# Kernel optimization log

Measured on AMD Instinct MI355X. Metric: run time of the kernel, lower is better.

Reference implementation:

```python
import jax, jax.numpy as jnp
import numpy as np

B, S, IN, OUT = 16, 512, 512, 256
D, H, L, DFF = 1024, 16, 6, 2048
HD = D // H
SCALE = HD ** -0.5
HID = 256  # fc1/fc2 hidden size


def setup_inputs() -> dict:
    key = jax.random.key(0)
    ks = jax.random.split(key, 40)
    g = lambda i, shape, s=0.02: (jax.random.normal(ks[i], shape, jnp.float32) * s)
    z = lambda shape: jnp.zeros(shape, jnp.float32)
    o = lambda shape: jnp.ones(shape, jnp.float32)
    vec = jnp.zeros((B, S), jnp.int32).at[:, 0].set(1)  # one-hot rows (assert-only arg)
    return {
        "x": jax.random.normal(ks[0], (B, S, IN), jnp.float32),
        "xm": jax.random.uniform(ks[1], (B, S), jnp.float32),
        "vecSelector": vec,
        "proj_w": g(2, (IN, D)), "proj_b": z((D,)),
        "pos": g(3, (S, D)),
        "qw": g(4, (L, D, D)), "qb": z((L, D)),
        "kw": g(5, (L, D, D)), "kb": z((L, D)),
        "vw": g(6, (L, D, D)), "vb": z((L, D)),
        "ow": g(7, (L, D, D)), "ob": z((L, D)),
        "ln1_g": o((L, D)), "ln1_b": z((L, D)),
        "ln2_g": o((L, D)), "ln2_b": z((L, D)),
        "w1": g(8, (L, D, DFF)), "b1": z((L, DFF)),
        "w2": g(9, (L, DFF, D)), "b2": z((L, D)),
        "fc1_w": g(10, (D, HID)), "fc1_b": z((HID,)),
        "fc2_w": g(11, (HID, HID)), "fc2_b": z((HID,)),
        "fc3_w": g(12, (HID, OUT)), "fc3_b": z((OUT,)),
    }


def _ln(x, g, b, eps=1e-5):
    m = jnp.mean(x, -1, keepdims=True)
    v = jnp.mean((x - m) ** 2, -1, keepdims=True)
    return (x - m) * jax.lax.rsqrt(v + eps) * g + b


def reference(x, xm, vecSelector, proj_w, proj_b, pos, qw, qb, kw, kb, vw, vb,
              ow, ob, ln1_g, ln1_b, ln2_g, ln2_b, w1, b1, w2, b2,
              fc1_w, fc1_b, fc2_w, fc2_b, fc3_w, fc3_b):
    # linear_proj + positional encoding (pos[:, :d_model] == pos)
    h = x @ proj_w + proj_b + pos  # (B,S,D)
    # key padding mask: whole batch rows masked where xm.sum(-1)==0
    skpm = jnp.broadcast_to((jnp.sum(xm, -1) == 0)[:, None], (B, S))  # (B,S) bool
    neg_inf = jnp.float32(-jnp.inf)
    for i in range(L):
        q = (h @ qw[i] + qb[i]) * SCALE
        k = h @ kw[i] + kb[i]
        v = h @ vw[i] + vb[i]
        q = q.reshape(B, S, H, HD)
        k = k.reshape(B, S, H, HD)
        v = v.reshape(B, S, H, HD)
        sc = jnp.einsum('bthd,bshd->bhts', q, k)  # (B,H,T,S)
        sc = jnp.where(skpm[:, None, None, :], neg_inf, sc)
        # safe_softmax: clamp to [-10,10] THEN softmax (-inf -> -10)
        aw = jax.nn.softmax(jnp.clip(sc, -10.0, 10.0), axis=-1)
        ao = jnp.einsum('bhts,bshd->bthd', aw, v).reshape(B, S, D)
        ao = ao @ ow[i] + ob[i]
        # forward hook: clamp + softmax over embed dim
        ao = jax.nn.softmax(jnp.clip(ao, -10.0, 10.0), axis=-1)
        # torch _sa_block's `[0]` slices batch dim of the raw tensor -> (S,D),
        # broadcast-added to every batch row
        sa = ao[0]
        h = _ln(h + sa[None, :, :], ln1_g[i], ln1_b[i])
        ff = jax.nn.relu(h @ w1[i] + b1[i]) @ w2[i] + b2[i]
        h = _ln(h + ff, ln2_g[i], ln2_b[i])
    out = h @ fc1_w + fc1_b
    for _ in range(5):
        out = out @ fc2_w + fc2_b
    out = out @ fc3_w + fc3_b  # (B,S,OUT)
    return out
```

## Files before the change

### kernel.cpp

```cpp
#include <hip/hip_runtime.h>
#include <hip/hip_bf16.h>

using bf16 = __hip_bfloat16;
typedef __attribute__((ext_vector_type(8))) short short8v;
typedef __attribute__((ext_vector_type(4))) float floatx4;

constexpr int Bc = 16, Sc = 512, INc = 512, OUTc = 256;
constexpr int Dc = 1024, Hc = 16, Lc = 6, DFFc = 2048, HIDc = 256;
constexpr float SCALEc = 0.125f;
constexpr int QKVS = 3072;

__device__ inline ushort f2b(float f) {
    union { float f; unsigned u; } v; v.f = f;
    unsigned r = (v.u + 0x7FFF + ((v.u >> 16) & 1)) >> 16;
    return (ushort)r;
}
__device__ inline float b2f(ushort b) {
    union { unsigned u; float f; } v; v.u = ((unsigned)b) << 16;
    return v.f;
}
__device__ inline float ldf(const float* p) { return *p; }
__device__ inline float ldf(const ushort* p) { return b2f(*p); }

__device__ inline void gll16(const ushort* g, ushort* l) {
    __builtin_amdgcn_global_load_lds(
        (const __attribute__((address_space(1))) unsigned int*)g,
        (__attribute__((address_space(3))) unsigned int*)l, 16, 0, 0);
}

__device__ inline float blockSum256(float v) {
    __shared__ float tmp[4];
#pragma unroll
    for (int o = 32; o > 0; o >>= 1) v += __shfl_xor(v, o, 64);
    int w = threadIdx.x >> 6;
    __syncthreads();
    if ((threadIdx.x & 63) == 0) tmp[w] = v;
    __syncthreads();
    return tmp[0] + tmp[1] + tmp[2] + tmp[3];
}
__device__ inline float blockMax256(float v) {
    __shared__ float tmp[4];
#pragma unroll
    for (int o = 32; o > 0; o >>= 1) v = fmaxf(v, __shfl_xor(v, o, 64));
    int w = threadIdx.x >> 6;
    __syncthreads();
    if ((threadIdx.x & 63) == 0) tmp[w] = v;
    __syncthreads();
    return fmaxf(fmaxf(tmp[0], tmp[1]), fmaxf(tmp[2], tmp[3]));
}

__global__ __launch_bounds__(256) void mask_k(const float* __restrict__ xm, float* __restrict__ flag) {
    float s = xm[threadIdx.x] + xm[threadIdx.x + 256];
    s = blockSum256(s);
    if (threadIdx.x == 0) flag[0] = (s == 0.f) ? 1.f : 0.f;
}

__global__ __launch_bounds__(256) void transp_k(const float* __restrict__ W, ushort* __restrict__ Wt,
                                                int K, int N, float wscale) {
    __shared__ float Ls[64][65];
    const int t = threadIdx.x;
    const int n0 = blockIdx.x * 64, k0 = blockIdx.y * 64;
    const int kr = t >> 4, n4 = (t & 15) * 4;
#pragma unroll
    for (int p = 0; p < 4; ++p) {
        float4 v = *(const float4*)&W[(size_t)(k0 + kr + p * 16) * N + n0 + n4];
        Ls[kr + p * 16][n4 + 0] = v.x; Ls[kr + p * 16][n4 + 1] = v.y;
        Ls[kr + p * 16][n4 + 2] = v.z; Ls[kr + p * 16][n4 + 3] = v.w;
    }
    __syncthreads();
    const int nr = t >> 4, k4 = (t & 15) * 4;
#pragma unroll
    for (int p = 0; p < 4; ++p) {
        ushort4 o;
        o.x = f2b(Ls[k4 + 0][nr + p * 16] * wscale); o.y = f2b(Ls[k4 + 1][nr + p * 16] * wscale);
        o.z = f2b(Ls[k4 + 2][nr + p * 16] * wscale); o.w = f2b(Ls[k4 + 3][nr + p * 16] * wscale);
        *(ushort4*)&Wt[(size_t)(n0 + nr + p * 16) * K + k0 + k4] = o;
    }
}

__global__ __launch_bounds__(256) void transp4_k(const float* __restrict__ qw, const float* __restrict__ kw,
                                                 const float* __restrict__ vw, const float* __restrict__ ow,
                                                 ushort* __restrict__ Wt) {
    const int z = blockIdx.z;
    const float* W = (z == 0) ? qw : (z == 1) ? kw : (z == 2) ? vw : ow;
    const float wscale = (z == 0) ? SCALEc : 1.f;
    ushort* dst = Wt + (size_t)z * Dc * Dc;
    __shared__ float Ls[64][65];
    const int t = threadIdx.x;
    const int n0 = blockIdx.x * 64, k0 = blockIdx.y * 64;
    const int kr = t >> 4, n4 = (t & 15) * 4;
#pragma unroll
    for (int p = 0; p < 4; ++p) {
        float4 v = *(const float4*)&W[(size_t)(k0 + kr + p * 16) * Dc + n0 + n4];
        Ls[kr + p * 16][n4 + 0] = v.x; Ls[kr + p * 16][n4 + 1] = v.y;
        Ls[kr + p * 16][n4 + 2] = v.z; Ls[kr + p * 16][n4 + 3] = v.w;
    }
    __syncthreads();
    const int nr = t >> 4, k4 = (t & 15) * 4;
#pragma unroll
    for (int p = 0; p < 4; ++p) {
        ushort4 o;
        o.x = f2b(Ls[k4 + 0][nr + p * 16] * wscale); o.y = f2b(Ls[k4 + 1][nr + p * 16] * wscale);
        o.z = f2b(Ls[k4 + 2][nr + p * 16] * wscale); o.w = f2b(Ls[k4 + 3][nr + p * 16] * wscale);
        *(ushort4*)&dst[(size_t)(n0 + nr + p * 16) * Dc + k0 + k4] = o;
    }
}

__device__ inline void ld16(const float* s, ushort* d) {
#pragma unroll
    for (int i = 0; i < 4; ++i) {
        float4 v = *(const float4*)(s + i * 4);
        d[i * 4 + 0] = f2b(v.x); d[i * 4 + 1] = f2b(v.y);
        d[i * 4 + 2] = f2b(v.z); d[i * 4 + 3] = f2b(v.w);
    }
}

template <typename TA, int ACT, bool ADDPOS, int OMODE>
__global__ __launch_bounds__(256) void mgemm_k(
    const TA* __restrict__ A, const ushort* __restrict__ Bt,
    const float* __restrict__ bias, const float* __restrict__ pos,
    float* __restrict__ Cf, ushort* __restrict__ Cb,
    int M, int N, int K, float scale)
{
    __shared__ __align__(16) ushort As[128 * 64];
    __shared__ __align__(16) ushort Bs[128 * 64];
    const int tid = threadIdx.x;
    const int nx = gridDim.x;
    const int nwg = nx * gridDim.y;
    int d = blockIdx.x + blockIdx.y * nx;
    if ((nwg & 7) == 0) d = (d & 7) * (nwg >> 3) + (d >> 3);
    const int m0 = (d / nx) * 128, n0 = (d % nx) * 128;
    const int lane = tid & 63, wv = tid >> 6;
    const int wm = (wv >> 1) * 64, wn = (wv & 1) * 64;
    floatx4 acc[4][4] = {};

    const int rA8 = lane >> 3, cch = lane & 7;
    const int srow = tid >> 2, scg = tid & 3;

    for (int k0 = 0; k0 < K; k0 += 64) {
#pragma unroll
        for (int p = 0; p < 4; ++p) {
            const int r = wv * 32 + p * 8 + rA8;
            const int cs = (cch ^ (r & 7)) * 8;
            gll16(&Bt[(size_t)(n0 + r) * K + k0 + cs], &Bs[(wv * 32 + p * 8) * 64]);
        }
        if constexpr (sizeof(TA) == 2) {
#pragma unroll
            for (int p = 0; p < 4; ++p) {
                const int r = wv * 32 + p * 8 + rA8;
                const int cs = (cch ^ (r & 7)) * 8;
                gll16((const ushort*)&A[(size_t)(m0 + r) * K + k0 + cs], &As[(wv * 32 + p * 8) * 64]);
            }
        } else {
#pragma unroll
            for (int p = 0; p < 2; ++p) {
                const int r = srow + p * 64;
                __align__(16) ushort ta[16];
                ld16(&A[(size_t)(m0 + r) * K + k0 + scg * 16], ta);
                const int base = r * 64, sw = (r & 7) * 8;
                *(short8v*)&As[base + ((scg * 16 + 0) ^ sw)] = *(short8v*)&ta[0];
                *(short8v*)&As[base + ((scg * 16 + 8) ^ sw)] = *(short8v*)&ta[8];
            }
        }
        __syncthreads();
#pragma unroll
        for (int s = 0; s < 2; ++s) {
            short8v af[4], bf_[4];
            const int kg = s * 32 + (lane >> 4) * 8;
#pragma unroll
            for (int f = 0; f < 4; ++f) {
                const int ra = wm + f * 16 + (lane & 15);
                af[f] = *(const short8v*)&As[ra * 64 + (kg ^ ((ra & 7) * 8))];
                const int rb = wn + f * 16 + (lane & 15);
                bf_[f] = *(const short8v*)&Bs[rb * 64 + (kg ^ ((rb & 7) * 8))];
            }
#pragma unroll
            for (int i = 0; i < 4; ++i)
#pragma unroll
                for (int j = 0; j < 4; ++j)
                    acc[i][j] = __builtin_amdgcn_mfma_f32_16x16x32_bf16(af[i], bf_[j], acc[i][j], 0, 0, 0);
        }
        __syncthreads();
    }

    const int cc = lane & 15, rr4 = (lane >> 4) * 4;
#pragma unroll
    for (int i = 0; i < 4; ++i) {
#pragma unroll
        for (int j = 0; j < 4; ++j) {
            const int col = n0 + wn + j * 16 + cc;
            const float bsv = bias[col];
#pragma unroll
            for (int q = 0; q < 4; ++q) {
                const int row = m0 + wm + i * 16 + rr4 + q;
                float v = acc[i][j][q] + bsv;
                if (ADDPOS) v += pos[(size_t)(row & (Sc - 1)) * N + col];
                v *= scale;
                if (ACT == 1) v = fmaxf(v, 0.f);
                if (OMODE == 0) Cf[(size_t)row * N + col] = v;
                else if (OMODE == 1) Cb[(size_t)row * N + col] = f2b(v);
                else { Cf[(size_t)row * N + col] = v; Cb[(size_t)row * N + col] = f2b(v); }
            }
        }
    }
}

__global__ __launch_bounds__(256) void fattn_k(
    const float* __restrict__ qkv, ushort* __restrict__ ao, const float* __restrict__ flag)
{
    const int hh = blockIdx.y;
    const int t0 = blockIdx.x * 32;
    __shared__ __align__(16) ushort Qs[32 * 64];
    __shared__ __align__(16) ushort Ks[64 * 64];
    __shared__ float Vs[64][68];
    __shared__ float Ps[32][68];
    __shared__ float rs[4][32];
    const int tid = threadIdx.x;
    const int lane = tid & 63, wv = tid >> 6;
    const bool msk = flag[0] > 0.5f;

    {
        const int r = tid >> 3, c = tid & 7;
        const float* src = &qkv[(size_t)(t0 + r) * QKVS + hh * 64 + c * 8];
        float4 v0 = *(const float4*)src, v1 = *(const float4*)(src + 4);
        __align__(16) ushort tmp[8] = {f2b(v0.x), f2b(v0.y), f2b(v0.z), f2b(v0.w),
                                       f2b(v1.x), f2b(v1.y), f2b(v1.z), f2b(v1.w)};
        *(short8v*)&Qs[r * 64 + ((c * 8) ^ ((r & 7) * 8))] = *(short8v*)tmp;
    }
    if (tid < 128) ((float*)rs)[tid] = 0.f;

    float o[8] = {};
    const int pq = tid >> 3, pd = (tid & 7) * 8;

    for (int s0 = 0; s0 < Sc; s0 += 64) {
        __syncthreads();
        {
            const int vr = tid >> 2, vc = (tid & 3) * 16;
            const float* vsrc = &qkv[(size_t)(s0 + vr) * QKVS + 2048 + hh * 64 + vc];
#pragma unroll
            for (int u = 0; u < 4; ++u)
                *(float4*)&Vs[vr][vc + u * 4] = *(const float4*)(vsrc + u * 4);
#pragma unroll
            for (int u = 0; u < 2; ++u) {
                const int task = tid + u * 256;
                const int kr = task >> 3, kc = task & 7;
                const float* ksrc = &qkv[(size_t)(s0 + kr) * QKVS + 1024 + hh * 64 + kc * 8];
                float4 a = *(const float4*)ksrc, b = *(const float4*)(ksrc + 4);
                __align__(16) ushort tmp[8] = {f2b(a.x), f2b(a.y), f2b(a.z), f2b(a.w),
                                               f2b(b.x), f2b(b.y), f2b(b.z), f2b(b.w)};
                *(short8v*)&Ks[kr * 64 + ((kc * 8) ^ ((kr & 7) * 8))] = *(short8v*)tmp;
            }
        }
        __syncthreads();
        floatx4 pacc[2] = {};
#pragma unroll
        for (int i = 0; i < 2; ++i)
#pragma unroll
            for (int s = 0; s < 2; ++s) {
                const int kg = s * 32 + (lane >> 4) * 8;
                const int ra = 16 * i + (lane & 15);
                short8v aq = *(const short8v*)&Qs[ra * 64 + (kg ^ ((ra & 7) * 8))];
                const int rb = 16 * wv + (lane & 15);
                short8v bk = *(const short8v*)&Ks[rb * 64 + (kg ^ ((rb & 7) * 8))];
                pacc[i] = __builtin_amdgcn_mfma_f32_16x16x32_bf16(aq, bk, pacc[i], 0, 0, 0);
            }
        const int cc = lane & 15, rr4 = (lane >> 4) * 4;
#pragma unroll
        for (int i = 0; i < 2; ++i)
#pragma unroll
            for (int q = 0; q < 4; ++q) {
                float v = fminf(fmaxf(pacc[i][q], -10.f), 10.f);
                if (msk) v = -10.f;
                float e = __expf(v - 10.f);
                Ps[16 * i + rr4 + q][wv * 16 + cc] = e;
                float rsum = e;
                rsum += __shfl_xor(rsum, 1, 64);
                rsum += __shfl_xor(rsum, 2, 64);
                rsum += __shfl_xor(rsum, 4, 64);
                rsum += __shfl_xor(rsum, 8, 64);
                if (cc == 0) rs[wv][16 * i + rr4 + q] += rsum;
            }
        __syncthreads();
#pragma unroll 8
        for (int ss = 0; ss < 64; ++ss) {
            float p = Ps[pq][ss];
#pragma unroll
            for (int u = 0; u < 8; ++u) o[u] += p * Vs[ss][pd + u];
        }
    }
    __syncthreads();
    float inv = 1.f / (rs[0][pq] + rs[1][pq] + rs[2][pq] + rs[3][pq]);
#pragma unroll
    for (int u = 0; u < 8; ++u)
        ao[(size_t)(t0 + pq) * Dc + hh * 64 + pd + u] = f2b(o[u] * inv);
}

template <typename TA, int ACT, bool ADDPOS, bool OUT_BF16, bool HASB>
__global__ __launch_bounds__(256) void gemm_k(
    const TA* __restrict__ A, const float* __restrict__ W,
    const float* __restrict__ bias, const float* __restrict__ pos,
    float* __restrict__ Cf, bf16* __restrict__ Cb,
    int M, int N, int K, float scale)
{
    __shared__ float As[16][68];
    __shared__ float Ws[16][68];
    const int tid = threadIdx.x;
    const int m0 = blockIdx.y * 64, n0 = blockIdx.x * 64;
    const int ty = tid >> 4, tx = tid & 15;
    float c[4][4] = {};

    const int ka = tid & 15, mb = tid >> 4;
    const int nw = tid & 63, kb = tid >> 6;

    for (int k0 = 0; k0 < K; k0 += 16) {
#pragma unroll
        for (int j = 0; j < 4; ++j) {
            int m = mb + 16 * j;
            As[ka][m] = ldf(&A[(size_t)(m0 + m) * K + k0 + ka]);
        }
#pragma unroll
        for (int j = 0; j < 4; ++j) {
            int k = kb + 4 * j;
            Ws[k][nw] = W[(size_t)(k0 + k) * N + n0 + nw];
        }
        __syncthreads();
#pragma unroll
        for (int k = 0; k < 16; ++k) {
            float4 av = *(const float4*)&As[k][ty * 4];
            float4 wv = *(const float4*)&Ws[k][tx * 4];
            float a[4] = {av.x, av.y, av.z, av.w};
            float w[4] = {wv.x, wv.y, wv.z, wv.w};
#pragma unroll
            for (int i = 0; i < 4; ++i)
#pragma unroll
                for (int j = 0; j < 4; ++j) c[i][j] += a[i] * w[j];
        }
        __syncthreads();
    }

#pragma unroll
    for (int i = 0; i < 4; ++i) {
        int m = m0 + ty * 4 + i;
#pragma unroll
        for (int j = 0; j < 4; ++j) {
            int n = n0 + tx * 4 + j;
            float v = c[i][j] + (HASB ? bias[n] : 0.f);
            if (ADDPOS) v += pos[(size_t)(m & (Sc - 1)) * N + n];
            v *= scale;
            if (ACT == 1) v = fmaxf(v, 0.f);
            if (OUT_BF16) Cb[(size_t)m * N + n] = __float2bfloat16(v);
            else          Cf[(size_t)m * N + n] = v;
        }
    }
}

__global__ __launch_bounds__(256) void biaschain_k(
    const float* __restrict__ fc1b, const float* __restrict__ fc2w, const float* __restrict__ fc2b,
    const float* __restrict__ fc3w, const float* __restrict__ fc3b, float* __restrict__ bc)
{
    __shared__ float vs[256];
    const int t = threadIdx.x;
    float v = fc1b[t];
    for (int r = 0; r < 5; ++r) {
        vs[t] = v; __syncthreads();
        float s = fc2b[t];
#pragma unroll 8
        for (int k = 0; k < 256; ++k) s += vs[k] * fc2w[k * 256 + t];
        v = s; __syncthreads();
    }
    vs[t] = v; __syncthreads();
    float s = fc3b[t];
#pragma unroll 8
    for (int k = 0; k < 256; ++k) s += vs[k] * fc3w[k * 256 + t];
    bc[t] = s;
}

__global__ __launch_bounds__(256) void qkvbias_k(
    const float* __restrict__ qb, const float* __restrict__ kb, const float* __restrict__ vb,
    float* __restrict__ o)
{
    int i = blockIdx.x * 256 + threadIdx.x;
    float v = (i < 1024) ? qb[i] * SCALEc : ((i < 2048) ? kb[i - 1024] : vb[i - 2048]);
    o[i] = v;
}

__global__ __launch_bounds__(256) void softmax_k(
    const float* __restrict__ in, float* __restrict__ out, int ncols, int doclip)
{
    const int row = blockIdx.x;
    const float* ip = in + (size_t)row * ncols;
    float* op = out + (size_t)row * ncols;
    const int nj = ncols >> 8;
    float r[4];
    float mx = -1e30f;
    for (int j = 0; j < nj; ++j) {
        float v = ip[threadIdx.x + 256 * j];
        if (doclip) v = fminf(fmaxf(v, -10.f), 10.f);
        r[j] = v;
        mx = fmaxf(mx, v);
    }
    mx = blockMax256(mx);
    float s = 0.f;
    for (int j = 0; j < nj; ++j) { r[j] = expf(r[j] - mx); s += r[j]; }
    s = blockSum256(s);
    float inv = 1.f / s;
    for (int j = 0; j < nj; ++j) op[threadIdx.x + 256 * j] = r[j] * inv;
}

template <bool BCAST, typename TADD>
__global__ __launch_bounds__(256) void add_ln_k(
    ushort* __restrict__ hb, const TADD* __restrict__ add,
    const float* __restrict__ g, const float* __restrict__ b)
{
    const int row = blockIdx.x;
    const TADD* ap = BCAST ? add + (size_t)(row & (Sc - 1)) * Dc : add + (size_t)row * Dc;
    ushort* hp = hb + (size_t)row * Dc;
    const int tid = threadIdx.x;
    const int c0 = tid * 4;
    ushort4 hv = *(const ushort4*)&hp[c0];
    float x[4] = {b2f(hv.x), b2f(hv.y), b2f(hv.z), b2f(hv.w)};
#pragma unroll
    for (int j = 0; j < 4; ++j) x[j] += ldf(&ap[c0 + j]);
    float s = x[0] + x[1] + x[2] + x[3];
    float mean = blockSum256(s) * (1.f / (float)Dc);
    float vsum = 0.f;
#pragma unroll
    for (int j = 0; j < 4; ++j) { float d = x[j] - mean; vsum += d * d; }
    float var = blockSum256(vsum) * (1.f / (float)Dc);
    float inv = rsqrtf(var + 1e-5f);
    float4 gv = *(const float4*)&g[c0];
    float4 bv = *(const float4*)&b[c0];
    ushort4 ov;
    ov.x = f2b((x[0] - mean) * inv * gv.x + bv.x);
    ov.y = f2b((x[1] - mean) * inv * gv.y + bv.y);
    ov.z = f2b((x[2] - mean) * inv * gv.z + bv.z);
    ov.w = f2b((x[3] - mean) * inv * gv.w + bv.w);
    *(ushort4*)&hp[c0] = ov;
}

extern "C" void kernel_launch(void* const* d_in, const int* in_sizes, int n_in,
                              void* d_out, int out_size, void* d_ws, size_t ws_size,
                              hipStream_t stream)
{
    const float* x      = (const float*)d_in[0];
    const float* xm     = (const float*)d_in[1];
    const float* proj_w = (const float*)d_in[3];
    const float* proj_b = (const float*)d_in[4];
    const float* pos    = (const float*)d_in[5];
    const float* qw     = (const float*)d_in[6];
    const float* qb     = (const float*)d_in[7];
    const float* kw     = (const float*)d_in[8];
    const float* kb     = (const float*)d_in[9];
    const float* vw     = (const float*)d_in[10];
    const float* vb     = (const float*)d_in[11];
    const float* ow     = (const float*)d_in[12];
    const float* obias  = (const float*)d_in[13];
    const float* ln1g   = (const float*)d_in[14];
    const float* ln1b   = (const float*)d_in[15];
    const float* ln2g   = (const float*)d_in[16];
    const float* ln2b   = (const float*)d_in[17];
    const float* w1     = (const float*)d_in[18];
    const float* b1     = (const float*)d_in[19];
    const float* w2     = (const float*)d_in[20];
    const float* b2     = (const float*)d_in[21];
    const float* fc1w   = (const float*)d_in[22];
    const float* fc1b   = (const float*)d_in[23];
    const float* fc2w   = (const float*)d_in[24];
    const float* fc2b   = (const float*)d_in[25];
    const float* fc3w   = (const float*)d_in[26];
    const float* fc3b   = (const float*)d_in[27];

    float* ws = (float*)d_ws;
    const size_t HSZ = (size_t)Bc * Sc * Dc;
    ushort* hb  = (ushort*)ws;
    ushort* ffu = (ushort*)(ws + HSZ / 2);
    float* rgA  = ws + HSZ;
    float* rgB  = ws + 2 * HSZ;
    float* flag = ws + 3 * HSZ;

    float* qkvf  = rgA;
    ushort* aovu = (ushort*)(rgA + 1572864);
    float* obv   = rgA + 1835008;
    float* qkvb  = rgA + 2359296;
    ushort* midu = (ushort*)rgA;

    ushort* Wt = (ushort*)rgB;

    float* W2  = rgA;
    float* W4  = rgA + 65536;
    float* W5  = rgA + 131072;
    float* C1  = rgA + 196608;
    float* Wc  = rgA + 458752;
    float* bcv = rgA + 720896;

    const int MR = Bc * Sc;

    mask_k<<<1, 256, 0, stream>>>(xm, flag);

    transp_k<<<dim3(Dc / 64, INc / 64), 256, 0, stream>>>(proj_w, Wt, INc, Dc, 1.f);
    mgemm_k<float, 0, true, 1><<<dim3(Dc / 128, MR / 128), 256, 0, stream>>>(
        x, Wt, proj_b, pos, nullptr, hb, MR, Dc, INc, 1.f);

    for (int l = 0; l < Lc; ++l) {
        const float* qw_l = qw + (size_t)l * Dc * Dc; const float* qb_l = qb + l * Dc;
        const float* kw_l = kw + (size_t)l * Dc * Dc; const float* kb_l = kb + l * Dc;
        const float* vw_l = vw + (size_t)l * Dc * Dc; const float* vb_l = vb + l * Dc;
        const float* ow_l = ow + (size_t)l * Dc * Dc; const float* ob_l = obias + l * Dc;
        const float* w1_l = w1 + (size_t)l * Dc * DFFc; const float* b1_l = b1 + l * DFFc;
        const float* w2_l = w2 + (size_t)l * DFFc * Dc; const float* b2_l = b2 + l * Dc;

        transp4_k<<<dim3(Dc / 64, Dc / 64, 4), 256, 0, stream>>>(qw_l, kw_l, vw_l, ow_l, Wt);
        qkvbias_k<<<12, 256, 0, stream>>>(qb_l, kb_l, vb_l, qkvb);
        mgemm_k<ushort, 0, false, 0><<<dim3(QKVS / 128, Sc / 128), 256, 0, stream>>>(
            hb, Wt, qkvb, nullptr, qkvf, nullptr, Sc, QKVS, Dc, 1.f);
        fattn_k<<<dim3(Sc / 32, Hc), 256, 0, stream>>>(qkvf, aovu, flag);
        mgemm_k<ushort, 0, false, 0><<<dim3(Dc / 128, Sc / 128), 256, 0, stream>>>(
            aovu, Wt + (size_t)3 * Dc * Dc, ob_l, nullptr, obv, nullptr, Sc, Dc, Dc, 1.f);
        softmax_k<<<Sc, 256, 0, stream>>>(obv, obv, Dc, 1);
        add_ln_k<true, float><<<MR, 256, 0, stream>>>(hb, obv, ln1g + l * Dc, ln1b + l * Dc);

        transp_k<<<dim3(DFFc / 64, Dc / 64), 256, 0, stream>>>(w1_l, Wt, Dc, DFFc, 1.f);
        mgemm_k<ushort, 1, false, 1><<<dim3(DFFc / 128, MR / 128), 256, 0, stream>>>(
            hb, Wt, b1_l, nullptr, nullptr, midu, MR, DFFc, Dc, 1.f);
        transp_k<<<dim3(Dc / 64, DFFc / 64), 256, 0, stream>>>(w2_l, Wt, DFFc, Dc, 1.f);
        mgemm_k<ushort, 0, false, 1><<<dim3(Dc / 128, MR / 128), 256, 0, stream>>>(
            midu, Wt, b2_l, nullptr, nullptr, ffu, MR, Dc, DFFc, 1.f);
        add_ln_k<false, ushort><<<MR, 256, 0, stream>>>(hb, ffu, ln2g + l * Dc, ln2b + l * Dc);
    }

    gemm_k<float, 0, false, false, false><<<dim3(4, 4), 256, 0, stream>>>(
        fc2w, fc2w, nullptr, nullptr, W2, nullptr, HIDc, HIDc, HIDc, 1.f);
    gemm_k<float, 0, false, false, false><<<dim3(4, 4), 256, 0, stream>>>(
        W2, W2, nullptr, nullptr, W4, nullptr, HIDc, HIDc, HIDc, 1.f);
    gemm_k<float, 0, false, false, false><<<dim3(4, 4), 256, 0, stream>>>(
        W4, fc2w, nullptr, nullptr, W5, nullptr, HIDc, HIDc, HIDc, 1.f);
    gemm_k<float, 0, false, false, false><<<dim3(4, 16), 256, 0, stream>>>(
        fc1w, W5, nullptr, nullptr, C1, nullptr, Dc, HIDc, HIDc, 1.f);
    gemm_k<float, 0, false, false, false><<<dim3(4, 16), 256, 0, stream>>>(
        C1, fc3w, nullptr, nullptr, Wc, nullptr, Dc, HIDc, HIDc, 1.f);
    biaschain_k<<<1, 256, 0, stream>>>(fc1b, fc2w, fc2b, fc3w, fc3b, bcv);
    transp_k<<<dim3(HIDc / 64, Dc / 64), 256, 0, stream>>>(Wc, Wt, Dc, HIDc, 1.f);
    mgemm_k<ushort, 0, false, 0><<<dim3(HIDc / 128, MR / 128), 256, 0, stream>>>(
        hb, Wt, bcv, nullptr, (float*)d_out, nullptr, MR, HIDc, Dc, 1.f);
}
```

Before: 1.403 ms.

## Batch all-layer weight transposes, bf16 QKV output, fuse softmax into add+LN

When the workspace is large enough, all six layers' weights are transposed to bf16 in one up-front launch, and the QKV biases for every layer are built in a single kernel. The QKV GEMM now writes bf16, so attention loads K/Q directly without converting. The output-projection softmax is folded into the residual add plus LayerNorm kernel. This cuts launch count, intermediate traffic and per-layer transpose overhead, at the cost of more workspace and a path that depends on the workspace size.

```diff
diff --git a/kernel.cpp b/kernel.cpp
--- a/kernel.cpp
+++ b/kernel.cpp
@@ -9,6 +9,7 @@
 constexpr int Dc = 1024, Hc = 16, Lc = 6, DFFc = 2048, HIDc = 256;
 constexpr float SCALEc = 0.125f;
 constexpr int QKVS = 3072;
+constexpr size_t LSLOT = 8388608;
 
 __device__ inline ushort f2b(float f) {
     union { float f; unsigned u; } v; v.f = f;
@@ -78,20 +79,31 @@
     }
 }
 
-__global__ __launch_bounds__(256) void transp4_k(const float* __restrict__ qw, const float* __restrict__ kw,
-                                                 const float* __restrict__ vw, const float* __restrict__ ow,
-                                                 ushort* __restrict__ Wt) {
+__global__ __launch_bounds__(256) void transpall_k(
+    const float* __restrict__ qw, const float* __restrict__ kw, const float* __restrict__ vw,
+    const float* __restrict__ ow, const float* __restrict__ w1, const float* __restrict__ w2,
+    ushort* __restrict__ Wt, int l0, size_t lstride)
+{
     const int z = blockIdx.z;
-    const float* W = (z == 0) ? qw : (z == 1) ? kw : (z == 2) ? vw : ow;
-    const float wscale = (z == 0) ? SCALEc : 1.f;
-    ushort* dst = Wt + (size_t)z * Dc * Dc;
+    const int l = l0 + z / 6, m = z % 6;
+    ushort* slot = Wt + (size_t)(z / 6) * lstride;
+    const float* W; ushort* dst; int K, N; float wscale = 1.f;
+    switch (m) {
+        case 0: W = qw + (size_t)l * Dc * Dc; K = Dc; N = Dc; dst = slot; wscale = SCALEc; break;
+        case 1: W = kw + (size_t)l * Dc * Dc; K = Dc; N = Dc; dst = slot + 1048576; break;
+        case 2: W = vw + (size_t)l * Dc * Dc; K = Dc; N = Dc; dst = slot + 2097152; break;
+        case 3: W = ow + (size_t)l * Dc * Dc; K = Dc; N = Dc; dst = slot + 3145728; break;
+        case 4: W = w1 + (size_t)l * Dc * DFFc; K = Dc; N = DFFc; dst = slot + 4194304; break;
+        default: W = w2 + (size_t)l * DFFc * Dc; K = DFFc; N = Dc; dst = slot + 6291456; break;
+    }
+    if (blockIdx.x >= N / 64 || blockIdx.y >= K / 64) return;
     __shared__ float Ls[64][65];
     const int t = threadIdx.x;
     const int n0 = blockIdx.x * 64, k0 = blockIdx.y * 64;
     const int kr = t >> 4, n4 = (t & 15) * 4;
 #pragma unroll
     for (int p = 0; p < 4; ++p) {
-        float4 v = *(const float4*)&W[(size_t)(k0 + kr + p * 16) * Dc + n0 + n4];
+        float4 v = *(const float4*)&W[(size_t)(k0 + kr + p * 16) * N + n0 + n4];
         Ls[kr + p * 16][n4 + 0] = v.x; Ls[kr + p * 16][n4 + 1] = v.y;
         Ls[kr + p * 16][n4 + 2] = v.z; Ls[kr + p * 16][n4 + 3] = v.w;
     }
@@ -102,7 +114,7 @@
         ushort4 o;
         o.x = f2b(Ls[k4 + 0][nr + p * 16] * wscale); o.y = f2b(Ls[k4 + 1][nr + p * 16] * wscale);
         o.z = f2b(Ls[k4 + 2][nr + p * 16] * wscale); o.w = f2b(Ls[k4 + 3][nr + p * 16] * wscale);
-        *(ushort4*)&dst[(size_t)(n0 + nr + p * 16) * Dc + k0 + k4] = o;
+        *(ushort4*)&dst[(size_t)(n0 + nr + p * 16) * K + k0 + k4] = o;
     }
 }
 
@@ -206,7 +218,7 @@
 }
 
 __global__ __launch_bounds__(256) void fattn_k(
-    const float* __restrict__ qkv, ushort* __restrict__ ao, const float* __restrict__ flag)
+    const ushort* __restrict__ qkv, ushort* __restrict__ ao, const float* __restrict__ flag)
 {
     const int hh = blockIdx.y;
     const int t0 = blockIdx.x * 32;
@@ -221,11 +233,8 @@
 
     {
         const int r = tid >> 3, c = tid & 7;
-        const float* src = &qkv[(size_t)(t0 + r) * QKVS + hh * 64 + c * 8];
-        float4 v0 = *(const float4*)src, v1 = *(const float4*)(src + 4);
-        __align__(16) ushort tmp[8] = {f2b(v0.x), f2b(v0.y), f2b(v0.z), f2b(v0.w),
-                                       f2b(v1.x), f2b(v1.y), f2b(v1.z), f2b(v1.w)};
-        *(short8v*)&Qs[r * 64 + ((c * 8) ^ ((r & 7) * 8))] = *(short8v*)tmp;
+        short8v q = *(const short8v*)&qkv[(size_t)(t0 + r) * QKVS + hh * 64 + c * 8];
+        *(short8v*)&Qs[r * 64 + ((c * 8) ^ ((r & 7) * 8))] = q;
     }
     if (tid < 128) ((float*)rs)[tid] = 0.f;
 
@@ -236,19 +245,19 @@
         __syncthreads();
         {
             const int vr = tid >> 2, vc = (tid & 3) * 16;
-            const float* vsrc = &qkv[(size_t)(s0 + vr) * QKVS + 2048 + hh * 64 + vc];
-#pragma unroll
-            for (int u = 0; u < 4; ++u)
-                *(float4*)&Vs[vr][vc + u * 4] = *(const float4*)(vsrc + u * 4);
+            const ushort* vsrc = &qkv[(size_t)(s0 + vr) * QKVS + 2048 + hh * 64 + vc];
+            short8v v0 = *(const short8v*)vsrc, v1 = *(const short8v*)(vsrc + 8);
+#pragma unroll
+            for (int u = 0; u < 8; ++u) {
+                Vs[vr][vc + u] = b2f((ushort)v0[u]);
+                Vs[vr][vc + 8 + u] = b2f((ushort)v1[u]);
+            }
 #pragma unroll
             for (int u = 0; u < 2; ++u) {
                 const int task = tid + u * 256;
                 const int kr = task >> 3, kc = task & 7;
-                const float* ksrc = &qkv[(size_t)(s0 + kr) * QKVS + 1024 + hh * 64 + kc * 8];
-                float4 a = *(const float4*)ksrc, b = *(const float4*)(ksrc + 4);
-                __align__(16) ushort tmp[8] = {f2b(a.x), f2b(a.y), f2b(a.z), f2b(a.w),
-                                               f2b(b.x), f2b(b.y), f2b(b.z), f2b(b.w)};
-                *(short8v*)&Ks[kr * 64 + ((kc * 8) ^ ((kr & 7) * 8))] = *(short8v*)tmp;
+                short8v kvv = *(const short8v*)&qkv[(size_t)(s0 + kr) * QKVS + 1024 + hh * 64 + kc * 8];
+                *(short8v*)&Ks[kr * 64 + ((kc * 8) ^ ((kr & 7) * 8))] = kvv;
             }
         }
         __syncthreads();
@@ -375,36 +384,55 @@
     bc[t] = s;
 }
 
-__global__ __launch_bounds__(256) void qkvbias_k(
+__global__ __launch_bounds__(256) void qkvbiasall_k(
     const float* __restrict__ qb, const float* __restrict__ kb, const float* __restrict__ vb,
     float* __restrict__ o)
 {
     int i = blockIdx.x * 256 + threadIdx.x;
-    float v = (i < 1024) ? qb[i] * SCALEc : ((i < 2048) ? kb[i - 1024] : vb[i - 2048]);
+    int l = i / QKVS, j = i - l * QKVS;
+    float v = (j < 1024) ? qb[l * Dc + j] * SCALEc
+            : (j < 2048) ? kb[l * Dc + j - 1024] : vb[l * Dc + j - 2048];
     o[i] = v;
 }
 
-__global__ __launch_bounds__(256) void softmax_k(
-    const float* __restrict__ in, float* __restrict__ out, int ncols, int doclip)
+__global__ __launch_bounds__(256) void smaddln_k(
+    ushort* __restrict__ hb, const float* __restrict__ obv,
+    const float* __restrict__ g, const float* __restrict__ b)
 {
     const int row = blockIdx.x;
-    const float* ip = in + (size_t)row * ncols;
-    float* op = out + (size_t)row * ncols;
-    const int nj = ncols >> 8;
-    float r[4];
+    const float* op = obv + (size_t)(row & (Sc - 1)) * Dc;
+    ushort* hp = hb + (size_t)row * Dc;
+    const int c0 = threadIdx.x * 4;
+    float4 ov = *(const float4*)&op[c0];
+    float r[4] = {ov.x, ov.y, ov.z, ov.w};
     float mx = -1e30f;
-    for (int j = 0; j < nj; ++j) {
-        float v = ip[threadIdx.x + 256 * j];
-        if (doclip) v = fminf(fmaxf(v, -10.f), 10.f);
-        r[j] = v;
-        mx = fmaxf(mx, v);
-    }
+#pragma unroll
+    for (int j = 0; j < 4; ++j) { r[j] = fminf(fmaxf(r[j], -10.f), 10.f); mx = fmaxf(mx, r[j]); }
     mx = blockMax256(mx);
     float s = 0.f;
-    for (int j = 0; j < nj; ++j) { r[j] = expf(r[j] - mx); s += r[j]; }
+#pragma unroll
+    for (int j = 0; j < 4; ++j) { r[j] = __expf(r[j] - mx); s += r[j]; }
     s = blockSum256(s);
-    float inv = 1.f / s;
-    for (int j = 0; j < nj; ++j) op[threadIdx.x + 256 * j] = r[j] * inv;
+    float sinv = 1.f / s;
+    ushort4 hv = *(const ushort4*)&hp[c0];
+    float x[4] = {b2f(hv.x), b2f(hv.y), b2f(hv.z), b2f(hv.w)};
+    float ssum = 0.f;
+#pragma unroll
+    for (int j = 0; j < 4; ++j) { x[j] += r[j] * sinv; ssum += x[j]; }
+    float mean = blockSum256(ssum) * (1.f / (float)Dc);
+    float vsum = 0.f;
+#pragma unroll
+    for (int j = 0; j < 4; ++j) { float d_ = x[j] - mean; vsum += d_ * d_; }
+    float var = blockSum256(vsum) * (1.f / (float)Dc);
+    float inv = rsqrtf(var + 1e-5f);
+    float4 gv = *(const float4*)&g[c0];
+    float4 bv = *(const float4*)&b[c0];
+    ushort4 o4;
+    o4.x = f2b((x[0] - mean) * inv * gv.x + bv.x);
+    o4.y = f2b((x[1] - mean) * inv * gv.y + bv.y);
+    o4.z = f2b((x[2] - mean) * inv * gv.z + bv.z);
+    o4.w = f2b((x[3] - mean) * inv * gv.w + bv.w);
+    *(ushort4*)&hp[c0] = o4;
 }
 
 template <bool BCAST, typename TADD>
@@ -415,8 +443,7 @@
     const int row = blockIdx.x;
     const TADD* ap = BCAST ? add + (size_t)(row & (Sc - 1)) * Dc : add + (size_t)row * Dc;
     ushort* hp = hb + (size_t)row * Dc;
-    const int tid = threadIdx.x;
-    const int c0 = tid * 4;
+    const int c0 = threadIdx.x * 4;
     ushort4 hv = *(const ushort4*)&hp[c0];
     float x[4] = {b2f(hv.x), b2f(hv.y), b2f(hv.z), b2f(hv.w)};
 #pragma unroll
@@ -474,18 +501,20 @@
     const size_t HSZ = (size_t)Bc * Sc * Dc;
     ushort* hb  = (ushort*)ws;
     ushort* ffu = (ushort*)(ws + HSZ / 2);
-    float* rgA  = ws + HSZ;
-    float* rgB  = ws + 2 * HSZ;
-    float* flag = ws + 3 * HSZ;
-
-    float* qkvf  = rgA;
-    ushort* aovu = (ushort*)(rgA + 1572864);
-    float* obv   = rgA + 1835008;
-    float* qkvb  = rgA + 2359296;
-    ushort* midu = (ushort*)rgA;
-
-    ushort* Wt = (ushort*)rgB;
-
+    float*  rgA = ws + HSZ;
+    float*  meta = ws + 2 * HSZ;
+    float*  flag = meta;
+    float*  qkvball = meta + 256;
+    ushort* Wt = (ushort*)(ws + 2 * HSZ + 262144);
+
+    const bool big = ws_size >= (size_t)163 * 1024 * 1024;
+    const size_t lstride = big ? LSLOT : 0;
+    ushort* projWt = big ? Wt + (size_t)6 * LSLOT : Wt;
+
+    ushort* qkvfu = (ushort*)rgA;
+    ushort* aovu  = (ushort*)(rgA + 786432);
+    float*  obv   = rgA + 1048576;
+    ushort* midu  = (ushort*)rgA;
     float* W2  = rgA;
     float* W4  = rgA + 65536;
     float* W5  = rgA + 131072;
@@ -496,35 +525,34 @@
     const int MR = Bc * Sc;
 
     mask_k<<<1, 256, 0, stream>>>(xm, flag);
-
-    transp_k<<<dim3(Dc / 64, INc / 64), 256, 0, stream>>>(proj_w, Wt, INc, Dc, 1.f);
+    qkvbiasall_k<<<72, 256, 0, stream>>>(qb, kb, vb, qkvball);
+    if (big)
+        transpall_k<<<dim3(32, 32, 36), 256, 0, stream>>>(qw, kw, vw, ow, w1, w2, Wt, 0, lstride);
+
+    transp_k<<<dim3(Dc / 64, INc / 64), 256, 0, stream>>>(proj_w, projWt, INc, Dc, 1.f);
     mgemm_k<float, 0, true, 1><<<dim3(Dc / 128, MR / 128), 256, 0, stream>>>(
-        x, Wt, proj_b, pos, nullptr, hb, MR, Dc, INc, 1.f);
+        x, projWt, proj_b, pos, nullptr, hb, MR, Dc, INc, 1.f);
 
     for (int l = 0; l < Lc; ++l) {
-        const float* qw_l = qw + (size_t)l * Dc * Dc; const float* qb_l = qb + l * Dc;
-        const float* kw_l = kw + (size_t)l * Dc * Dc; const float* kb_l = kb + l * Dc;
-        const float* vw_l = vw + (size_t)l * Dc * Dc; const float* vb_l = vb + l * Dc;
-        const float* ow_l = ow + (size_t)l * Dc * Dc; const float* ob_l = obias + l * Dc;
-        const float* w1_l = w1 + (size_t)l * Dc * DFFc; const float* b1_l = b1 + l * DFFc;
-        const float* w2_l = w2 + (size_t)l * DFFc * Dc; const float* b2_l = b2 + l * Dc;
-
-        transp4_k<<<dim3(Dc / 64, Dc / 64, 4), 256, 0, stream>>>(qw_l, kw_l, vw_l, ow_l, Wt);
-        qkvbias_k<<<12, 256, 0, stream>>>(qb_l, kb_l, vb_l, qkvb);
-        mgemm_k<ushort, 0, false, 0><<<dim3(QKVS / 128, Sc / 128), 256, 0, stream>>>(
-            hb, Wt, qkvb, nullptr, qkvf, nullptr, Sc, QKVS, Dc, 1.f);
-        fattn_k<<<dim3(Sc / 32, Hc), 256, 0, stream>>>(qkvf, aovu, flag);
+        ushort* slot = Wt + (size_t)(big ? l : 0) * LSLOT;
+        const float* ob_l = obias + l * Dc;
+        const float* b1_l = b1 + l * DFFc;
+        const float* b2_l = b2 + l * Dc;
+
+        if (!big)
+            transpall_k<<<dim3(32, 32, 6), 256, 0, stream>>>(qw, kw, vw, ow, w1, w2, Wt, l, 0);
+
+        mgemm_k<ushort, 0, false, 1><<<dim3(QKVS / 128, Sc / 128), 256, 0, stream>>>(
+            hb, slot, qkvball + l * QKVS, nullptr, nullptr, qkvfu, Sc, QKVS, Dc, 1.f);
+        fattn_k<<<dim3(Sc / 32, Hc), 256, 0, stream>>>(qkvfu, aovu, flag);
         mgemm_k<ushort, 0, false, 0><<<dim3(Dc / 128, Sc / 128), 256, 0, stream>>>(
-            aovu, Wt + (size_t)3 * Dc * Dc, ob_l, nullptr, obv, nullptr, Sc, Dc, Dc, 1.f);
-        softmax_k<<<Sc, 256, 0, stream>>>(obv, obv, Dc, 1);
-        add_ln_k<true, float><<<MR, 256, 0, stream>>>(hb, obv, ln1g + l * Dc, ln1b + l * Dc);
-
-        transp_k<<<dim3(DFFc / 64, Dc / 64), 256, 0, stream>>>(w1_l, Wt, Dc, DFFc, 1.f);
+            aovu, slot + 3145728, ob_l, nullptr, obv, nullptr, Sc, Dc, Dc, 1.f);
+        smaddln_k<<<MR, 256, 0, stream>>>(hb, obv, ln1g + l * Dc, ln1b + l * Dc);
+
         mgemm_k<ushort, 1, false, 1><<<dim3(DFFc / 128, MR / 128), 256, 0, stream>>>(
-            hb, Wt, b1_l, nullptr, nullptr, midu, MR, DFFc, Dc, 1.f);
-        transp_k<<<dim3(Dc / 64, DFFc / 64), 256, 0, stream>>>(w2_l, Wt, DFFc, Dc, 1.f);
+            hb, slot + 4194304, b1_l, nullptr, nullptr, midu, MR, DFFc, Dc, 1.f);
         mgemm_k<ushort, 0, false, 1><<<dim3(Dc / 128, MR / 128), 256, 0, stream>>>(
-            midu, Wt, b2_l, nullptr, nullptr, ffu, MR, Dc, DFFc, 1.f);
+            midu, slot + 6291456, b2_l, nullptr, nullptr, ffu, MR, Dc, DFFc, 1.f);
         add_ln_k<false, ushort><<<MR, 256, 0, stream>>>(hb, ffu, ln2g + l * Dc, ln2b + l * Dc);
     }
 
```

Measured after the change: 1.398 ms. Within noise of the previous version (-0.3%).
